# Kernel optimization log

Measured on AMD Instinct MI355X. Metric: run time of the kernel, lower is better.

## Reference

```python
import jax, jax.numpy as jnp
import numpy as np

B, STEP, H, N_ENC = 256, 32, 512, 60
PD, LD, NB, NTYPE, NPLAYER = 32, 32, 6, 11, 35


def _parity_masks(S):
    # Static relation-11/12 edge masks from update_adjacency_matrix (step is a Python int).
    m11 = np.zeros((S, S), dtype=bool)
    m12 = np.zeros((S, S), dtype=bool)
    for row in range(S):
        ni = row // 2
        if row % 2 == 0:
            c = (ni + 1) * 2
            if c <= S - 1:
                (m11 if ni % 2 == 0 else m12)[row, c] = True
                (m11 if ni % 2 == 0 else m12)[c, row] = True
        else:
            c = (ni + 1) * 2 + 1
            if c <= S - 1:
                (m12 if ni % 2 == 0 else m11)[row, c] = True
                (m12 if ni % 2 == 0 else m11)[c, row] = True
    return jnp.asarray(m11), jnp.asarray(m12)


def update_adjacency(adj, step, shot_type_predict=False):
    b = adj.shape[0]
    S = step * 2
    new = jnp.zeros((b, 13, S, S), dtype=adj.dtype).at[:, :, :S - 2, :S - 2].set(adj)
    m11, m12 = _parity_masks(S)
    new = new.at[:, 11].set(jnp.where(m11, 1, new[:, 11]))
    new = new.at[:, 12].set(jnp.where(m12, 1, new[:, 12]))
    if shot_type_predict:
        idx = (step - 1) * 2 if step % 2 == 0 else (step - 1) * 2 + 1
        new = new.at[:, :, idx, :].set(0).at[:, :, :, idx].set(0)
    return new


def rgcn(node, adj, layer_params):
    # adj: (B,13,N,N) int; slice off relation 0 -> 12 relations. Dropout is eval-mode identity.
    adj_f = adj[:, 1:].astype(node.dtype)  # (B,12,N,N)
    x = node
    n_layers = len(layer_params)
    for i, (basis, comb, w_self) in enumerate(layer_params):
        act = jax.nn.sigmoid if i == n_layers - 1 else jax.nn.relu
        W = jnp.einsum('rb,bij->rij', comb, basis)            # (12,H,H)
        msg = jnp.einsum('brnm,bmh->brnh', adj_f, x)          # (B,12,N,H)
        x = act(jnp.einsum('brnh,rhk->bnk', msg, W) + x @ w_self.T)
    return x


def setup_inputs() -> dict:
    key = jax.random.key(0)
    ks = jax.random.split(key, 20)
    s = 0.05
    return {
        'player': jax.random.randint(ks[0], (B, 2), 0, NPLAYER, dtype=jnp.int32),
        'step': STEP,
        'encode_node_embedding': jax.random.normal(ks[1], (B, N_ENC, H), jnp.float32),
        'adjacency_matrix': jax.random.randint(ks[2], (B, 13, (STEP - 1) * 2, (STEP - 1) * 2), 0, 2, dtype=jnp.int32),
        'player_A_x': jax.random.uniform(ks[3], (B, 1), jnp.float32),
        'player_A_y': jax.random.uniform(ks[4], (B, 1), jnp.float32),
        'player_B_x': jax.random.uniform(ks[5], (B, 1), jnp.float32),
        'player_B_y': jax.random.uniform(ks[6], (B, 1), jnp.float32),
        'emb_table': jax.random.normal(ks[7], (NPLAYER, PD), jnp.float32) * s,
        'coord_W': jax.random.normal(ks[8], (LD, 2), jnp.float32) * s,
        'coord_b': jnp.zeros((LD,), jnp.float32),
        'in_W': jax.random.normal(ks[9], (H, PD + LD), jnp.float32) * s,
        'in_b': jnp.zeros((H,), jnp.float32),
        'basis0': jax.random.normal(ks[10], (NB, H, H), jnp.float32) * s,
        'comb0': jax.random.normal(ks[11], (12, NB), jnp.float32) * s,
        'self0': jax.random.normal(ks[12], (H, H), jnp.float32) * s,
        'basis1': jax.random.normal(ks[13], (NB, H, H), jnp.float32) * s,
        'comb1': jax.random.normal(ks[14], (12, NB), jnp.float32) * s,
        'self1': jax.random.normal(ks[15], (H, H), jnp.float32) * s,
        'type_W': jax.random.normal(ks[16], (NTYPE, 2 * H), jnp.float32) * s,
        'type_b': jnp.zeros((NTYPE,), jnp.float32),
    }


def reference(player, step, encode_node_embedding, adjacency_matrix,
              player_A_x, player_A_y, player_B_x, player_B_y,
              emb_table, coord_W, coord_b, in_W, in_b,
              basis0, comb0, self0, basis1, comb1, self1, type_W, type_b):
    b = player.shape[0]
    layers = [(basis0, comb0, self0), (basis1, comb1, self1)]

    coord_A = jnp.stack([player_A_x, player_A_y], axis=2)   # (B,1,2)
    coord_B = jnp.stack([player_B_x, player_B_y], axis=2)   # (B,1,2)
    coords = jnp.stack([coord_A, coord_B], axis=2).reshape(b, -1, 2)  # (B,2,2)
    loc = jax.nn.relu(coords @ coord_W.T + coord_b)          # (B,2,LD)
    pemb = emb_table[player]                                 # (B,2,PD)
    initial = jnp.concatenate([loc, pemb], axis=-1) @ in_W.T + in_b  # (B,2,H)

    # first=False branch: current coords == prev coords, so model_input == initial
    mi = jnp.concatenate([encode_node_embedding, initial], axis=1)   # (B,62,H)
    tmp = rgcn(mi, adjacency_matrix, layers)
    passed = jnp.concatenate([encode_node_embedding[:, :-2], tmp[:, -4:]], axis=1)  # (B,62,H)

    tmp_adj = update_adjacency(adjacency_matrix, step, shot_type_predict=True)  # (B,13,64,64)
    mi2 = jnp.concatenate([passed, initial], axis=1)         # (B,64,H)
    drop = (step - 1) * 2 if step % 2 == 0 else (step - 1) * 2 + 1
    keep = np.delete(np.arange(step * 2), drop)
    mi2 = mi2[:, keep]
    tmp_adj = tmp_adj[:, :, keep][:, :, :, keep]
    tmp2 = rgcn(mi2, tmp_adj, layers)                        # (B,63,H)

    pad = jnp.zeros((b, tmp2.shape[1] + 1, tmp2.shape[2]), tmp2.dtype)
    if step % 2 == 0:
        pad = pad.at[:, :-2].set(tmp2[:, :-1]).at[:, -1].set(tmp2[:, -1])
    else:
        pad = pad.at[:, :-1].set(tmp2)
    stp = jnp.concatenate([passed[:, :-2], pad[:, -4:]], axis=1)  # (B,64,H)
    if step % 2 == 0:
        black = stp[:, (step - 1) * 2 + 1]
        white = stp[:, (step - 2) * 2]
    else:
        black = stp[:, (step - 2) * 2 + 1]
        white = stp[:, (step - 1) * 2]
    logits = jnp.concatenate([black, white], axis=-1) @ type_W.T + type_b
    return logits
```

## Files before the change

kernel.cpp:

```cpp
#include <hip/hip_runtime.h>
#include <hip/hip_bf16.h>

typedef unsigned short u16;
typedef unsigned long long u64;
typedef __attribute__((ext_vector_type(4))) short short4v;
typedef __attribute__((ext_vector_type(8))) short short8;
typedef __attribute__((ext_vector_type(4))) float floatx4;

__device__ __forceinline__ u16 f2bf(float f) {
    union { float f; unsigned u; } v; v.f = f;
    unsigned r = v.u + 0x7FFF + ((v.u >> 16) & 1);
    return (u16)(r >> 16);
}

__global__ void k_wcat(const float* __restrict__ basis, const float* __restrict__ selfW,
                       u16* __restrict__ wf) {
    int bi = blockIdx.x, t = threadIdx.x;
    int kr = t >> 7;
    int nb = (t & 127) * 4;
    for (int it = 0; it < 4; ++it) {
        int k = bi * 8 + it * 2 + kr;
        float v0, v1, v2, v3;
        if (k < 3072) {
            int q = k >> 9, h = k & 511;
            const float4 bz = *(const float4*)(basis + ((size_t)(q * 512 + h)) * 512 + nb);
            v0 = bz.x; v1 = bz.y; v2 = bz.z; v3 = bz.w;
        } else {
            int kk = k - 3072;
            v0 = selfW[(size_t)(nb + 0) * 512 + kk];
            v1 = selfW[(size_t)(nb + 1) * 512 + kk];
            v2 = selfW[(size_t)(nb + 2) * 512 + kk];
            v3 = selfW[(size_t)(nb + 3) * 512 + kk];
        }
        float vv[4] = {v0, v1, v2, v3};
        for (int i = 0; i < 4; ++i) {
            int n = nb + i;
            wf[(size_t)(k >> 5) * 16384 + (n >> 4) * 512 + ((k >> 3) & 3) * 128 + (n & 15) * 8 + (k & 7)] = f2bf(vv[i]);
        }
    }
}

__global__ void k_masks(const int* __restrict__ A, u64* __restrict__ m0, u64* __restrict__ m1) {
    int bi = blockIdx.x;
    int b = bi / 12, r = bi % 12;
    const int* Ab = A + (size_t)(b * 13 + (r + 1)) * 62 * 62;
    int lane = threadIdx.x;
    u64 my0 = 0, my1 = 0;
    for (int n = 0; n < 64; ++n) {
        int raw = 0;
        if (n < 62 && lane < 62) raw = (Ab[n * 62 + lane] != 0) ? 1 : 0;
        u64 b0 = __ballot(raw != 0);
        int v1 = 0;
        if (n < 63 && lane < 63) {
            int oi = (n == 62) ? 63 : n;
            int oj = (lane == 62) ? 63 : lane;
            v1 = (oi < 62 && oj < 62) ? raw : 0;
            int lo = (oi < oj) ? oi : oj, hi = (oi < oj) ? oj : oi;
            if (hi == lo + 2) {
                int p = (lo >> 1) & 1;
                int chp = ((lo & 1) == 0) ? (p ? 12 : 11) : (p ? 11 : 12);
                if (r + 1 == chp) v1 = 1;
            }
        }
        u64 b1 = __ballot(v1 != 0);
        if (lane == n) { my0 = b0; my1 = b1; }
    }
    m0[(size_t)bi * 64 + lane] = my0;
    m1[(size_t)bi * 64 + lane] = my1;
}

#define AQ_SETSTRIDE (256UL * 6 * 4096)
__global__ void k_aqexp(const u64* __restrict__ msk, const float* __restrict__ comb0,
                        const float* __restrict__ comb1, u16* __restrict__ aq) {
    int b = blockIdx.x >> 3, sp = blockIdx.x & 7;
    int t = threadIdx.x;
    __shared__ u64 sm[12 * 64];
    __shared__ float cmb[2][12][6];
    if (t < 72) { cmb[0][t / 6][t % 6] = comb0[t]; cmb[1][t / 6][t % 6] = comb1[t]; }
    for (int i = t; i < 768; i += 256) sm[i] = msk[(size_t)b * 768 + i];
    __syncthreads();
    #pragma unroll
    for (int ii2 = 0; ii2 < 2; ++ii2) {
        int pos = (sp * 2 + ii2) * 256 + t;
        int f = pos >> 9, lane = (pos >> 3) & 63, j = pos & 7;
        int row = ((f >> 1) << 4) + (lane & 15);
        int mb  = ((f & 1) << 5) + ((lane >> 4) << 3) + j;
        float bits[12];
        #pragma unroll
        for (int r = 0; r < 12; ++r) bits[r] = (float)((sm[r * 64 + row] >> mb) & 1ull);
        #pragma unroll
        for (int s = 0; s < 2; ++s)
            #pragma unroll
            for (int q = 0; q < 6; ++q) {
                float v = 0.f;
                #pragma unroll
                for (int r = 0; r < 12; ++r) v += bits[r] * cmb[s][r][q];
                aq[(size_t)s * AQ_SETSTRIDE + ((size_t)b * 6 + q) * 4096 + pos] = f2bf(v);
            }
    }
}

__global__ void k_prep(const int* __restrict__ player,
                       const float* __restrict__ pAx, const float* __restrict__ pAy,
                       const float* __restrict__ pBx, const float* __restrict__ pBy,
                       const float* __restrict__ emb, const float* __restrict__ cW,
                       const float* __restrict__ cb, const float* __restrict__ inW,
                       const float* __restrict__ inb,
                       u16* __restrict__ mi1, u16* __restrict__ mi2) {
    int b = blockIdx.x, t = threadIdx.x;
    __shared__ float feat[2][64];
    if (t < 64) {
        int j = t >> 5, d = t & 31;
        float X = j ? pBx[b] : pAx[b];
        float Y = j ? pBy[b] : pAy[b];
        feat[j][d] = fmaxf(cW[d * 2] * X + cW[d * 2 + 1] * Y + cb[d], 0.f);
        feat[j][32 + d] = emb[player[b * 2 + j] * 32 + d];
    }
    __syncthreads();
    for (int h = t; h < 512; h += 256) {
        float a0 = inb[h], a1 = inb[h];
        const float* wrow = inW + h * 64;
        #pragma unroll
        for (int d = 0; d < 64; ++d) {
            float wv = wrow[d];
            a0 += wv * feat[0][d];
            a1 += wv * feat[1][d];
        }
        u16 v0 = f2bf(a0), v1 = f2bf(a1);
        size_t base = (size_t)b * 64 * 512;
        mi1[base + 60 * 512 + h] = v0;
        mi1[base + 61 * 512 + h] = v1;
        mi1[base + 62 * 512 + h] = 0;
        mi1[base + 63 * 512 + h] = 0;
        mi2[base + 62 * 512 + h] = v1;
        mi2[base + 63 * 512 + h] = 0;
    }
}

__global__ void k_cast(const float* __restrict__ enc, u16* __restrict__ mi1, u16* __restrict__ mi2) {
    long long e = ((long long)blockIdx.x * 256 + threadIdx.x) * 8;
    if (e >= 256LL * 60 * 512) return;
    int b = (int)(e / (60 * 512));
    int rm = (int)(e % (60 * 512));
    int n = rm / 512, h = rm % 512;
    for (int i = 0; i < 8; ++i) {
        u16 v = f2bf(enc[e + i]);
        mi1[((size_t)b * 64 + n) * 512 + h + i] = v;
        if (n < 58) mi2[((size_t)b * 64 + n) * 512 + h + i] = v;
    }
}

__global__ __launch_bounds__(512, 2)
void k_layer(const u16* __restrict__ x, const u16* __restrict__ aq,
             const u16* __restrict__ wc, u16* __restrict__ out) {
    int b = blockIdx.x;
    int t = threadIdx.x, lane = t & 63, w = t >> 6;
    int l15 = lane & 15, lq = lane >> 4;
    const int TS = 520;
    __shared__ __align__(16) u16 T[64 * 520];

    const u16* xb_base = x + (size_t)b * 64 * 512;
    short8 xb[8];
    #pragma unroll
    for (int nt = 0; nt < 4; ++nt)
        #pragma unroll
        for (int kh = 0; kh < 2; ++kh) {
            int h = (w * 4 + nt) * 16 + l15;
            int j0 = kh * 32 + lq * 8;
            short8 v;
            #pragma unroll
            for (int jj = 0; jj < 8; ++jj)
                v[jj] = (short)xb_base[(size_t)(j0 + jj) * 512 + h];
            xb[nt * 2 + kh] = v;
        }

    floatx4 acc[16];
    #pragma unroll
    for (int i = 0; i < 16; ++i) acc[i] = (floatx4)(0.f);

    const u16* aqb   = aq + (size_t)b * 6 * 4096 + (size_t)lane * 8;
    const u16* wbase = wc + (size_t)lane * 8;

    for (int q = 0; q < 6; ++q) {
        __syncthreads();
        for (int i = 0; i < 4; ++i) {
            short8 a0 = *(const short8*)(aqb + (size_t)q * 4096 + (i * 2 + 0) * 512);
            short8 a1 = *(const short8*)(aqb + (size_t)q * 4096 + (i * 2 + 1) * 512);
            #pragma unroll
            for (int nt = 0; nt < 4; ++nt) {
                floatx4 tz = (floatx4)(0.f);
                tz = __builtin_amdgcn_mfma_f32_16x16x32_bf16(a0, xb[nt * 2 + 0], tz, 0, 0, 0);
                tz = __builtin_amdgcn_mfma_f32_16x16x32_bf16(a1, xb[nt * 2 + 1], tz, 0, 0, 0);
                int hcol = (w * 4 + nt) * 16 + l15;
                int mrow = i * 16 + lq * 4;
                #pragma unroll
                for (int reg = 0; reg < 4; ++reg)
                    T[(mrow + reg) * TS + hcol] = f2bf(tz[reg]);
            }
        }
        __syncthreads();
        for (int ks = 0; ks < 16; ++ks) {
            short8 af[4], bf[4];
            #pragma unroll
            for (int i = 0; i < 4; ++i)
                af[i] = *(const short8*)&T[(i * 16 + l15) * TS + ks * 32 + lq * 8];
            #pragma unroll
            for (int nt = 0; nt < 4; ++nt)
                bf[nt] = *(const short8*)(wbase + (size_t)(q * 16 + ks) * 16384 + (size_t)(w * 4 + nt) * 512);
            #pragma unroll
            for (int i = 0; i < 4; ++i)
                #pragma unroll
                for (int nt = 0; nt < 4; ++nt)
                    acc[i * 4 + nt] = __builtin_amdgcn_mfma_f32_16x16x32_bf16(af[i], bf[nt], acc[i * 4 + nt], 0, 0, 0);
        }
    }
    for (int ks = 0; ks < 16; ++ks) {
        short8 af[4], bf[4];
        #pragma unroll
        for (int i = 0; i < 4; ++i)
            af[i] = *(const short8*)(xb_base + (size_t)(i * 16 + l15) * 512 + ks * 32 + lq * 8);
        #pragma unroll
        for (int nt = 0; nt < 4; ++nt)
            bf[nt] = *(const short8*)(wbase + (size_t)(96 + ks) * 16384 + (size_t)(w * 4 + nt) * 512);
        #pragma unroll
        for (int i = 0; i < 4; ++i)
            #pragma unroll
            for (int nt = 0; nt < 4; ++nt)
                acc[i * 4 + nt] = __builtin_amdgcn_mfma_f32_16x16x32_bf16(af[i], bf[nt], acc[i * 4 + nt], 0, 0, 0);
    }
    #pragma unroll
    for (int i = 0; i < 4; ++i)
        #pragma unroll
        for (int nt = 0; nt < 4; ++nt) {
            int n = (w * 4 + nt) * 16 + l15;
            int m0 = i * 16 + lq * 4;
            #pragma unroll
            for (int reg = 0; reg < 4; ++reg)
                out[((size_t)b * 64 + m0 + reg) * 512 + n] = f2bf(fmaxf(acc[i * 4 + nt][reg], 0.f));
        }
}

__global__ __launch_bounds__(512, 2)
void k_layer_last(const u16* __restrict__ x, const u16* __restrict__ aq,
                  const u16* __restrict__ wc, int mode,
                  u16* __restrict__ o16, float* __restrict__ o32) {
    int b = blockIdx.x;
    int t = threadIdx.x, lane = t & 63, w = t >> 6;
    int l15 = lane & 15, lq = lane >> 4;
    const int TS = 520;
    __shared__ __align__(16) u16 T[16 * 520];

    const u16* xb_base = x + (size_t)b * 64 * 512;
    short8 xb[8];
    #pragma unroll
    for (int nt = 0; nt < 4; ++nt)
        #pragma unroll
        for (int kh = 0; kh < 2; ++kh) {
            int h = (w * 4 + nt) * 16 + l15;
            int j0 = kh * 32 + lq * 8;
            short8 v;
            #pragma unroll
            for (int jj = 0; jj < 8; ++jj)
                v[jj] = (short)xb_base[(size_t)(j0 + jj) * 512 + h];
            xb[nt * 2 + kh] = v;
        }

    floatx4 acc[4];
    #pragma unroll
    for (int i = 0; i < 4; ++i) acc[i] = (floatx4)(0.f);

    const u16* aqb   = aq + (size_t)b * 6 * 4096 + (size_t)lane * 8;
    const u16* wbase = wc + (size_t)lane * 8;

    for (int q = 0; q < 6; ++q) {
        __syncthreads();
        {
            short8 a0 = *(const short8*)(aqb + (size_t)q * 4096 + 6 * 512);
            short8 a1 = *(const short8*)(aqb + (size_t)q * 4096 + 7 * 512);
            #pragma unroll
            for (int nt = 0; nt < 4; ++nt) {
                floatx4 tz = (floatx4)(0.f);
                tz = __builtin_amdgcn_mfma_f32_16x16x32_bf16(a0, xb[nt * 2 + 0], tz, 0, 0, 0);
                tz = __builtin_amdgcn_mfma_f32_16x16x32_bf16(a1, xb[nt * 2 + 1], tz, 0, 0, 0);
                int hcol = (w * 4 + nt) * 16 + l15;
                int mrow = lq * 4;
                #pragma unroll
                for (int reg = 0; reg < 4; ++reg)
                    T[(mrow + reg) * TS + hcol] = f2bf(tz[reg]);
            }
        }
        __syncthreads();
        for (int ks = 0; ks < 16; ++ks) {
            short8 af = *(const short8*)&T[l15 * TS + ks * 32 + lq * 8];
            #pragma unroll
            for (int nt = 0; nt < 4; ++nt) {
                short8 bf = *(const short8*)(wbase + (size_t)(q * 16 + ks) * 16384 + (size_t)(w * 4 + nt) * 512);
                acc[nt] = __builtin_amdgcn_mfma_f32_16x16x32_bf16(af, bf, acc[nt], 0, 0, 0);
            }
        }
    }
    for (int ks = 0; ks < 16; ++ks) {
        short8 af = *(const short8*)(xb_base + (size_t)(48 + l15) * 512 + ks * 32 + lq * 8);
        #pragma unroll
        for (int nt = 0; nt < 4; ++nt) {
            short8 bf = *(const short8*)(wbase + (size_t)(96 + ks) * 16384 + (size_t)(w * 4 + nt) * 512);
            acc[nt] = __builtin_amdgcn_mfma_f32_16x16x32_bf16(af, bf, acc[nt], 0, 0, 0);
        }
    }
    #pragma unroll
    for (int nt = 0; nt < 4; ++nt) {
        int n = (w * 4 + nt) * 16 + l15;
        #pragma unroll
        for (int reg = 0; reg < 4; ++reg) {
            int m = 48 + lq * 4 + reg;
            float v = acc[nt][reg];
            if (mode == 1) {
                if (m >= 58 && m <= 61)
                    o16[((size_t)b * 64 + m) * 512 + n] = f2bf(1.f / (1.f + __expf(-v)));
            } else {
                if (m == 60 || m == 62) {
                    int slot = (m == 60) ? (b * 2) : (b * 2 + 1);
                    o32[(size_t)slot * 512 + n] = 1.f / (1.f + __expf(-v));
                }
            }
        }
    }
}

__global__ void k_final(const float* __restrict__ t2, const float* __restrict__ tW,
                        const float* __restrict__ tb, float* __restrict__ outp) {
    int b = blockIdx.x, l = threadIdx.x;
    float a[11];
    #pragma unroll
    for (int j = 0; j < 11; ++j) a[j] = 0.f;
    for (int it = 0; it < 16; ++it) {
        int h = it * 64 + l;
        float c = (h < 512) ? t2[(b * 2 + 1) * 512 + h] : t2[(b * 2 + 0) * 512 + (h - 512)];
        #pragma unroll
        for (int j = 0; j < 11; ++j) a[j] += c * tW[j * 1024 + h];
    }
    #pragma unroll
    for (int j = 0; j < 11; ++j) {
        float v = a[j];
        for (int off = 32; off > 0; off >>= 1) v += __shfl_down(v, off, 64);
        if (l == 0) outp[b * 11 + j] = v + tb[j];
    }
}

extern "C" void kernel_launch(void* const* d_in, const int* in_sizes, int n_in,
                              void* d_out, int out_size, void* d_ws, size_t ws_size,
                              hipStream_t stream) {
    const int*   player = (const int*)d_in[0];
    const float* enc    = (const float*)d_in[2];
    const int*   adjm   = (const int*)d_in[3];
    const float* pAx    = (const float*)d_in[4];
    const float* pAy    = (const float*)d_in[5];
    const float* pBx    = (const float*)d_in[6];
    const float* pBy    = (const float*)d_in[7];
    const float* emb    = (const float*)d_in[8];
    const float* cW     = (const float*)d_in[9];
    const float* cb     = (const float*)d_in[10];
    const float* inW    = (const float*)d_in[11];
    const float* inb    = (const float*)d_in[12];
    const float* basis0 = (const float*)d_in[13];
    const float* comb0  = (const float*)d_in[14];
    const float* self0  = (const float*)d_in[15];
    const float* basis1 = (const float*)d_in[16];
    const float* comb1  = (const float*)d_in[17];
    const float* self1  = (const float*)d_in[18];
    const float* typeW  = (const float*)d_in[19];
    const float* typeb  = (const float*)d_in[20];

    char* ws = (char*)d_ws;
    size_t off = 0;
    auto alloc = [&](size_t bytes) -> void* {
        void* p = ws + off;
        off = (off + bytes + 255) & ~(size_t)255;
        return p;
    };
    u16* mi1   = (u16*)alloc(256UL * 64 * 512 * 2);
    u16* mi2   = (u16*)alloc(256UL * 64 * 512 * 2);
    u16* x12   = (u16*)alloc(256UL * 64 * 512 * 2);
    u16* aqbuf = (u16*)alloc(2UL * AQ_SETSTRIDE * 2);
    u16* wcat0 = (u16*)alloc(3584UL * 512 * 2);
    u16* wcat1 = (u16*)alloc(3584UL * 512 * 2);
    u64* mm0   = (u64*)alloc(256UL * 12 * 64 * 8);
    u64* mm1   = (u64*)alloc(256UL * 12 * 64 * 8);
    u16* x12b  = mi1;
    float* t2  = (float*)x12;
    u16* aq0   = aqbuf;
    u16* aq1   = aqbuf + AQ_SETSTRIDE;

    k_wcat<<<448, 256, 0, stream>>>(basis0, self0, wcat0);
    k_wcat<<<448, 256, 0, stream>>>(basis1, self1, wcat1);
    k_masks<<<3072, 64, 0, stream>>>(adjm, mm0, mm1);
    k_aqexp<<<2048, 256, 0, stream>>>(mm0, comb0, comb1, aqbuf);
    k_prep<<<256, 256, 0, stream>>>(player, pAx, pAy, pBx, pBy, emb, cW, cb, inW, inb, mi1, mi2);
    k_cast<<<3840, 256, 0, stream>>>(enc, mi1, mi2);

    k_layer<<<256, 512, 0, stream>>>(mi1, aq0, wcat0, x12);
    k_layer_last<<<256, 512, 0, stream>>>(x12, aq1, wcat1, 1, mi2, nullptr);
    k_aqexp<<<2048, 256, 0, stream>>>(mm1, comb0, comb1, aqbuf);
    k_layer<<<256, 512, 0, stream>>>(mi2, aq0, wcat0, x12b);
    k_layer_last<<<256, 512, 0, stream>>>(x12b, aq1, wcat1, 2, nullptr, t2);

    k_final<<<256, 64, 0, stream>>>(t2, typeW, typeb, (float*)d_out);
}
```

Before: 624.4 us.

## Double-buffer adjacency-message tile in LDS and vectorize input cast

The layer kernels now keep two LDS buffers for the per-relation-group message tile. The next group's adjacency×x product is computed while the current group's weight GEMM runs, and the self-weight GEMM is moved before the loop to overlap with the first stage. This halves the barriers per iteration and hides the message computation behind MFMA work. In exchange LDS doubles (about 133KB for k_layer) and launch bounds drop to one block per CU, which lowers occupancy. The cast kernel also now uses float4 loads and 16-byte packed bf16 stores instead of scalar element loops.

```diff
diff --git a/kernel.cpp b/kernel.cpp
--- a/kernel.cpp
+++ b/kernel.cpp
@@ -143,21 +143,25 @@
     int b = (int)(e / (60 * 512));
     int rm = (int)(e % (60 * 512));
     int n = rm / 512, h = rm % 512;
-    for (int i = 0; i < 8; ++i) {
-        u16 v = f2bf(enc[e + i]);
-        mi1[((size_t)b * 64 + n) * 512 + h + i] = v;
-        if (n < 58) mi2[((size_t)b * 64 + n) * 512 + h + i] = v;
-    }
-}
-
-__global__ __launch_bounds__(512, 2)
+    float4 f0 = *(const float4*)(enc + e);
+    float4 f1 = *(const float4*)(enc + e + 4);
+    short8 pk;
+    pk[0] = (short)f2bf(f0.x); pk[1] = (short)f2bf(f0.y);
+    pk[2] = (short)f2bf(f0.z); pk[3] = (short)f2bf(f0.w);
+    pk[4] = (short)f2bf(f1.x); pk[5] = (short)f2bf(f1.y);
+    pk[6] = (short)f2bf(f1.z); pk[7] = (short)f2bf(f1.w);
+    *(short8*)(mi1 + ((size_t)b * 64 + n) * 512 + h) = pk;
+    if (n < 58) *(short8*)(mi2 + ((size_t)b * 64 + n) * 512 + h) = pk;
+}
+
+__global__ __launch_bounds__(512, 1)
 void k_layer(const u16* __restrict__ x, const u16* __restrict__ aq,
              const u16* __restrict__ wc, u16* __restrict__ out) {
     int b = blockIdx.x;
     int t = threadIdx.x, lane = t & 63, w = t >> 6;
     int l15 = lane & 15, lq = lane >> 4;
     const int TS = 520;
-    __shared__ __align__(16) u16 T[64 * 520];
+    __shared__ __align__(16) u16 T[2][64 * 520];
 
     const u16* xb_base = x + (size_t)b * 64 * 512;
     short8 xb[8];
@@ -181,11 +185,11 @@
     const u16* aqb   = aq + (size_t)b * 6 * 4096 + (size_t)lane * 8;
     const u16* wbase = wc + (size_t)lane * 8;
 
-    for (int q = 0; q < 6; ++q) {
-        __syncthreads();
+    auto stageA = [&](int qq, u16* buf) {
+        #pragma unroll
         for (int i = 0; i < 4; ++i) {
-            short8 a0 = *(const short8*)(aqb + (size_t)q * 4096 + (i * 2 + 0) * 512);
-            short8 a1 = *(const short8*)(aqb + (size_t)q * 4096 + (i * 2 + 1) * 512);
+            short8 a0 = *(const short8*)(aqb + (size_t)qq * 4096 + (i * 2 + 0) * 512);
+            short8 a1 = *(const short8*)(aqb + (size_t)qq * 4096 + (i * 2 + 1) * 512);
             #pragma unroll
             for (int nt = 0; nt < 4; ++nt) {
                 floatx4 tz = (floatx4)(0.f);
@@ -195,15 +199,36 @@
                 int mrow = i * 16 + lq * 4;
                 #pragma unroll
                 for (int reg = 0; reg < 4; ++reg)
-                    T[(mrow + reg) * TS + hcol] = f2bf(tz[reg]);
+                    buf[(mrow + reg) * TS + hcol] = f2bf(tz[reg]);
             }
         }
-        __syncthreads();
+    };
+
+    stageA(0, T[0]);
+    for (int ks = 0; ks < 16; ++ks) {
+        short8 af[4], bf[4];
+        #pragma unroll
+        for (int i = 0; i < 4; ++i)
+            af[i] = *(const short8*)(xb_base + (size_t)(i * 16 + l15) * 512 + ks * 32 + lq * 8);
+        #pragma unroll
+        for (int nt = 0; nt < 4; ++nt)
+            bf[nt] = *(const short8*)(wbase + (size_t)(96 + ks) * 16384 + (size_t)(w * 4 + nt) * 512);
+        #pragma unroll
+        for (int i = 0; i < 4; ++i)
+            #pragma unroll
+            for (int nt = 0; nt < 4; ++nt)
+                acc[i * 4 + nt] = __builtin_amdgcn_mfma_f32_16x16x32_bf16(af[i], bf[nt], acc[i * 4 + nt], 0, 0, 0);
+    }
+    __syncthreads();
+
+    for (int q = 0; q < 6; ++q) {
+        int cur = q & 1;
+        if (q < 5) stageA(q + 1, T[cur ^ 1]);
         for (int ks = 0; ks < 16; ++ks) {
             short8 af[4], bf[4];
             #pragma unroll
             for (int i = 0; i < 4; ++i)
-                af[i] = *(const short8*)&T[(i * 16 + l15) * TS + ks * 32 + lq * 8];
+                af[i] = *(const short8*)&T[cur][(i * 16 + l15) * TS + ks * 32 + lq * 8];
             #pragma unroll
             for (int nt = 0; nt < 4; ++nt)
                 bf[nt] = *(const short8*)(wbase + (size_t)(q * 16 + ks) * 16384 + (size_t)(w * 4 + nt) * 512);
@@ -213,21 +238,9 @@
                 for (int nt = 0; nt < 4; ++nt)
                     acc[i * 4 + nt] = __builtin_amdgcn_mfma_f32_16x16x32_bf16(af[i], bf[nt], acc[i * 4 + nt], 0, 0, 0);
         }
-    }
-    for (int ks = 0; ks < 16; ++ks) {
-        short8 af[4], bf[4];
-        #pragma unroll
-        for (int i = 0; i < 4; ++i)
-            af[i] = *(const short8*)(xb_base + (size_t)(i * 16 + l15) * 512 + ks * 32 + lq * 8);
-        #pragma unroll
-        for (int nt = 0; nt < 4; ++nt)
-            bf[nt] = *(const short8*)(wbase + (size_t)(96 + ks) * 16384 + (size_t)(w * 4 + nt) * 512);
-        #pragma unroll
-        for (int i = 0; i < 4; ++i)
-            #pragma unroll
-            for (int nt = 0; nt < 4; ++nt)
-                acc[i * 4 + nt] = __builtin_amdgcn_mfma_f32_16x16x32_bf16(af[i], bf[nt], acc[i * 4 + nt], 0, 0, 0);
-    }
+        __syncthreads();
+    }
+
     #pragma unroll
     for (int i = 0; i < 4; ++i)
         #pragma unroll
@@ -240,7 +253,7 @@
         }
 }
 
-__global__ __launch_bounds__(512, 2)
+__global__ __launch_bounds__(512, 1)
 void k_layer_last(const u16* __restrict__ x, const u16* __restrict__ aq,
                   const u16* __restrict__ wc, int mode,
                   u16* __restrict__ o16, float* __restrict__ o32) {
@@ -248,7 +261,7 @@
     int t = threadIdx.x, lane = t & 63, w = t >> 6;
     int l15 = lane & 15, lq = lane >> 4;
     const int TS = 520;
-    __shared__ __align__(16) u16 T[16 * 520];
+    __shared__ __align__(16) u16 T[2][16 * 520];
 
     const u16* xb_base = x + (size_t)b * 64 * 512;
     short8 xb[8];
@@ -272,41 +285,47 @@
     const u16* aqb   = aq + (size_t)b * 6 * 4096 + (size_t)lane * 8;
     const u16* wbase = wc + (size_t)lane * 8;
 
+    auto stageA = [&](int qq, u16* buf) {
+        short8 a0 = *(const short8*)(aqb + (size_t)qq * 4096 + 6 * 512);
+        short8 a1 = *(const short8*)(aqb + (size_t)qq * 4096 + 7 * 512);
+        #pragma unroll
+        for (int nt = 0; nt < 4; ++nt) {
+            floatx4 tz = (floatx4)(0.f);
+            tz = __builtin_amdgcn_mfma_f32_16x16x32_bf16(a0, xb[nt * 2 + 0], tz, 0, 0, 0);
+            tz = __builtin_amdgcn_mfma_f32_16x16x32_bf16(a1, xb[nt * 2 + 1], tz, 0, 0, 0);
+            int hcol = (w * 4 + nt) * 16 + l15;
+            int mrow = lq * 4;
+            #pragma unroll
+            for (int reg = 0; reg < 4; ++reg)
+                buf[(mrow + reg) * TS + hcol] = f2bf(tz[reg]);
+        }
+    };
+
+    stageA(0, T[0]);
+    for (int ks = 0; ks < 16; ++ks) {
+        short8 af = *(const short8*)(xb_base + (size_t)(48 + l15) * 512 + ks * 32 + lq * 8);
+        #pragma unroll
+        for (int nt = 0; nt < 4; ++nt) {
+            short8 bf = *(const short8*)(wbase + (size_t)(96 + ks) * 16384 + (size_t)(w * 4 + nt) * 512);
+            acc[nt] = __builtin_amdgcn_mfma_f32_16x16x32_bf16(af, bf, acc[nt], 0, 0, 0);
+        }
+    }
+    __syncthreads();
+
     for (int q = 0; q < 6; ++q) {
-        __syncthreads();
-        {
-            short8 a0 = *(const short8*)(aqb + (size_t)q * 4096 + 6 * 512);
-            short8 a1 = *(const short8*)(aqb + (size_t)q * 4096 + 7 * 512);
-            #pragma unroll
-            for (int nt = 0; nt < 4; ++nt) {
-                floatx4 tz = (floatx4)(0.f);
-                tz = __builtin_amdgcn_mfma_f32_16x16x32_bf16(a0, xb[nt * 2 + 0], tz, 0, 0, 0);
-                tz = __builtin_amdgcn_mfma_f32_16x16x32_bf16(a1, xb[nt * 2 + 1], tz, 0, 0, 0);
-                int hcol = (w * 4 + nt) * 16 + l15;
-                int mrow = lq * 4;
-                #pragma unroll
-                for (int reg = 0; reg < 4; ++reg)
-                    T[(mrow + reg) * TS + hcol] = f2bf(tz[reg]);
-            }
-        }
-        __syncthreads();
+        int cur = q & 1;
+        if (q < 5) stageA(q + 1, T[cur ^ 1]);
         for (int ks = 0; ks < 16; ++ks) {
-            short8 af = *(const short8*)&T[l15 * TS + ks * 32 + lq * 8];
+            short8 af = *(const short8*)&T[cur][l15 * TS + ks * 32 + lq * 8];
             #pragma unroll
             for (int nt = 0; nt < 4; ++nt) {
                 short8 bf = *(const short8*)(wbase + (size_t)(q * 16 + ks) * 16384 + (size_t)(w * 4 + nt) * 512);
                 acc[nt] = __builtin_amdgcn_mfma_f32_16x16x32_bf16(af, bf, acc[nt], 0, 0, 0);
             }
         }
-    }
-    for (int ks = 0; ks < 16; ++ks) {
-        short8 af = *(const short8*)(xb_base + (size_t)(48 + l15) * 512 + ks * 32 + lq * 8);
-        #pragma unroll
-        for (int nt = 0; nt < 4; ++nt) {
-            short8 bf = *(const short8*)(wbase + (size_t)(96 + ks) * 16384 + (size_t)(w * 4 + nt) * 512);
-            acc[nt] = __builtin_amdgcn_mfma_f32_16x16x32_bf16(af, bf, acc[nt], 0, 0, 0);
-        }
-    }
+        __syncthreads();
+    }
+
     #pragma unroll
     for (int nt = 0; nt < 4; ++nt) {
         int n = (w * 4 + nt) * 16 + l15;
```

New measurement: 715.2 us. 1.15x slower.
